# Kernel optimization log

Measured on AMD Instinct MI355X. Metric: run time of the kernel, lower is better.

## Reference

```python
import jax, jax.numpy as jnp
import numpy as np

B, N, DIM, HEADS = 8, 4096, 512, 8
BASE = 10000.0


def rope_cos_sin(n, dim, base=BASE):
    k_max = dim // 2
    theta = 1.0 / base ** (jnp.arange(k_max, dtype=jnp.float32) / k_max)
    angles = jnp.arange(n, dtype=jnp.float32)[:, None] * theta  # (n, k_max)
    return jnp.cos(angles), jnp.sin(angles)


def apply_rope(x, cos, sin):
    # x: (b, n, dim); complex pairs are interleaved (even=real, odd=imag)
    xr = x[..., 0::2]
    xi = x[..., 1::2]
    out_r = cos * xr - sin * xi
    out_i = sin * xr + cos * xi
    return jnp.stack([out_r, out_i], axis=-1).reshape(x.shape)


def setup_inputs() -> dict:
    key = jax.random.key(0)
    ks = jax.random.split(key, 8)
    s = 0.02
    return {
        'x': jax.random.normal(ks[0], (B, N, DIM), jnp.float32),
        'y': jax.random.normal(ks[1], (B, N, DIM), jnp.float32),
        'Wq': jax.random.normal(ks[2], (DIM, DIM), jnp.float32) * s,
        'bq': jax.random.normal(ks[3], (DIM,), jnp.float32) * s,
        'Wk': jax.random.normal(ks[4], (DIM, DIM), jnp.float32) * s,
        'bk': jax.random.normal(ks[5], (DIM,), jnp.float32) * s,
        'lepe_w': jax.random.normal(ks[6], (DIM, 1, 3), jnp.float32) * s,
        'lepe_b': jax.random.normal(ks[7], (DIM,), jnp.float32) * s,
    }


def reference(x, y, Wq, bq, Wk, bk, lepe_w, lepe_b):
    b, n, c = x.shape
    h = HEADS
    d = c // h
    q = jax.nn.elu(x @ Wq.T + bq) + 1.0
    k = jax.nn.elu(y @ Wk.T + bk) + 1.0
    cos, sin = rope_cos_sin(n, c)
    q_rope = apply_rope(q, cos, sin).reshape(b, n, h, d).transpose(0, 2, 1, 3)
    k_rope = apply_rope(k, cos, sin).reshape(b, n, h, d).transpose(0, 2, 1, 3)
    qh = q.reshape(b, n, h, d).transpose(0, 2, 1, 3)
    kh = k.reshape(b, n, h, d).transpose(0, 2, 1, 3)
    v = y.reshape(b, n, h, d).transpose(0, 2, 1, 3)
    kmean = kh.mean(axis=2, keepdims=True)  # (b,h,1,d)
    z = 1.0 / (jnp.einsum('bhnd,bhmd->bhnm', qh, kmean) + 1e-6)  # (b,h,n,1)
    scale = n ** (-0.5)
    kv = jnp.einsum('bhnd,bhne->bhde', k_rope * scale, v * scale)  # (b,h,d,d)
    out = jnp.einsum('bhnd,bhde->bhne', q_rope, kv) * z  # (b,h,n,d)
    out = out.transpose(0, 2, 1, 3).reshape(b, n, c)
    # LePE: depthwise conv1d over value stream
    vc = v.transpose(0, 2, 1, 3).reshape(b, n, c).transpose(0, 2, 1)  # (b,c,n)
    lepe = jax.lax.conv_general_dilated(
        vc, lepe_w, window_strides=(1,), padding=[(1, 1)],
        dimension_numbers=('NCH', 'OIH', 'NCH'), feature_group_count=c)
    lepe = lepe + lepe_b[None, :, None]
    return out + lepe.transpose(0, 2, 1)
```

## Files before the change

kernel.cpp:

```cpp
#include <hip/hip_runtime.h>

#define B_ 8
#define N_ 4096
#define C_ 512
#define H_ 8

typedef _Float16 h8  __attribute__((ext_vector_type(8)));
typedef _Float16 h4v __attribute__((ext_vector_type(4)));
typedef float    f4  __attribute__((ext_vector_type(4)));

static const size_t OFF_COS  = 0;
static const size_t OFF_SIN  = (size_t)4*1024*1024;
static const size_t OFF_KRH  = (size_t)8*1024*1024;
static const size_t OFF_YH   = (size_t)40*1024*1024;
static const size_t OFF_WQH  = (size_t)72*1024*1024;
static const size_t OFF_WKH  = (size_t)72*1024*1024 + 512*1024;
static const size_t OFF_KSUM = (size_t)73*1024*1024;
static const size_t OFF_KVG  = (size_t)73*1024*1024 + 64*1024;
static const size_t OFF_KVT  = (size_t)74*1024*1024 + 64*1024;

__device__ __forceinline__ unsigned int pack2h(float a, float b){
    union { _Float16 h[2]; unsigned int u; } x;
    x.h[0] = (_Float16)a; x.h[1] = (_Float16)b; return x.u;
}

__global__ void k_tables(float* __restrict__ cosT, float* __restrict__ sinT){
    int n = blockIdx.x, j = threadIdx.x;
    double th = exp((double)j * -0.035977892078031970);
    float ang = (float)n * (float)th;
    float s, c; sincosf(ang, &s, &c);
    cosT[n*256 + j] = c; sinT[n*256 + j] = s;
}

__global__ __launch_bounds__(256) void k_prep_y(
    const float* __restrict__ y, const float* __restrict__ Wq, const float* __restrict__ Wk,
    _Float16* __restrict__ yh, _Float16* __restrict__ Wqh, _Float16* __restrict__ Wkh)
{
    int bid = blockIdx.x;
    const float* src; _Float16* dst; size_t base;
    if (bid < 8192)      { src = y;  dst = yh;  base = (size_t)bid*2048; }
    else if (bid < 8320) { src = Wq; dst = Wqh; base = (size_t)(bid-8192)*2048; }
    else                 { src = Wk; dst = Wkh; base = (size_t)(bid-8320)*2048; }
    size_t o = base + (size_t)threadIdx.x*8;
    float4 a = *(const float4*)&src[o];
    float4 b = *(const float4*)&src[o+4];
    uint4 r; r.x = pack2h(a.x,a.y); r.y = pack2h(a.z,a.w); r.z = pack2h(b.x,b.y); r.w = pack2h(b.z,b.w);
    *(uint4*)&dst[o] = r;
}

__global__ __launch_bounds__(256) void k_prep_x(const float* __restrict__ x, _Float16* __restrict__ xh){
    size_t o = (size_t)blockIdx.x*2048 + (size_t)threadIdx.x*8;
    float4 a = *(const float4*)&x[o];
    float4 b = *(const float4*)&x[o+4];
    uint4 r; r.x = pack2h(a.x,a.y); r.y = pack2h(a.z,a.w); r.z = pack2h(b.x,b.y); r.w = pack2h(b.z,b.w);
    *(uint4*)&xh[o] = r;
}

__device__ __forceinline__ void stage_a64(const _Float16* __restrict__ g, _Float16* lds, int t){
    int r = t >> 2;
    int j = (t & 3) ^ ((r ^ (r >> 2)) & 3);
    __builtin_amdgcn_global_load_lds(
        (const __attribute__((address_space(1))) void*)(g + (size_t)r*C_ + j*8),
        (__attribute__((address_space(3))) void*)(lds + (size_t)(t & 192)*8),
        16, 0, 0);
}
__device__ __forceinline__ void stage_b128(const _Float16* __restrict__ g, _Float16* lds, int t){
#pragma unroll
    for (int i=0;i<2;++i){
        int u = i*256 + t;
        int r = u >> 2;
        int j = (u & 3) ^ ((r ^ (r >> 2)) & 3);
        __builtin_amdgcn_global_load_lds(
            (const __attribute__((address_space(1))) void*)(g + (size_t)r*C_ + j*8),
            (__attribute__((address_space(3))) void*)(lds + (size_t)(i*256 + (t & 192))*8),
            16, 0, 0);
    }
}

template<int IS_Q>
__global__ __launch_bounds__(256, 4) void k_gemm(
    const _Float16* __restrict__ A, const _Float16* __restrict__ Wh, const float* __restrict__ bias,
    const float* __restrict__ cosT, const float* __restrict__ sinT,
    _Float16* __restrict__ krh, float* __restrict__ ksum,
    const float* __restrict__ ksumIn, const _Float16* __restrict__ kvTg,
    const _Float16* __restrict__ yh, const float* __restrict__ lw, const float* __restrict__ lb,
    float* __restrict__ outp)
{
    __shared__ __align__(16) char smem[36864];
    _Float16* qrs = (_Float16*)smem;

    const int t = threadIdx.x;
    const int lane = t & 63;
    const int w = t >> 6;
    const int wm = w >> 1, wn = w & 1;
    const int col0 = blockIdx.x * 128;
    const int row0 = blockIdx.y * 64;
    const int lrow = lane & 15, lg = lane >> 4;
    const int b = row0 >> 12;

    f4 acc[2][4] = {};
    const _Float16* Ab = A  + (size_t)row0*C_;
    const _Float16* Bb = Wh + (size_t)col0*C_;
    stage_a64 (Ab,      (_Float16*)(smem),               t);
    stage_b128(Bb,      (_Float16*)(smem + 12288),       t);
    stage_a64 (Ab + 32, (_Float16*)(smem + 4096),        t);
    stage_b128(Bb + 32, (_Float16*)(smem + 12288 + 8192),t);

    const int sw = (lrow ^ (lrow >> 2)) & 3;
    const int cK = (lg ^ sw) * 8;

#pragma unroll
    for (int kk=0; kk<16; ++kk){
        if (kk < 15) asm volatile("s_waitcnt vmcnt(3)" ::: "memory");
        else         asm volatile("s_waitcnt vmcnt(0)" ::: "memory");
        __builtin_amdgcn_s_barrier();
        if (kk < 14){
            const int ss = (kk+2)%3;
            stage_a64 (Ab + (kk+2)*32, (_Float16*)(smem + ss*4096),         t);
            stage_b128(Bb + (kk+2)*32, (_Float16*)(smem + 12288 + ss*8192), t);
        }
        const int sc = kk%3;
        const _Float16* As = (const _Float16*)(smem + sc*4096);
        const _Float16* Bs = (const _Float16*)(smem + 12288 + sc*8192);
        h8 af[2], bf[4];
#pragma unroll
        for (int mi=0; mi<2; ++mi) af[mi] = *(const h8*)&As[(wm*32 + mi*16 + lrow)*32 + cK];
#pragma unroll
        for (int ni=0; ni<4; ++ni) bf[ni] = *(const h8*)&Bs[(wn*64 + ni*16 + lrow)*32 + cK];
#pragma unroll
        for (int mi=0; mi<2; ++mi)
#pragma unroll
            for (int ni=0; ni<4; ++ni)
                acc[mi][ni] = __builtin_amdgcn_mfma_f32_16x16x32_f16(af[mi], bf[ni], acc[mi][ni], 0,0,0);
    }
    __syncthreads();

    const int hcol0 = col0 + wn*64;
    float bcol[4], km[4];
#pragma unroll
    for (int ni=0; ni<4; ++ni){
        int c = hcol0 + ni*16 + lrow;
        bcol[ni] = bias[c];
        km[ni] = IS_Q ? ksumIn[b*C_ + c] * (1.0f/4096.0f) : 0.0f;
    }
    float colsum[4] = {0.f,0.f,0.f,0.f};
    float zr[2][4];
    _Float16* qw = qrs + w*2304;

#pragma unroll
    for (int mi=0; mi<2; ++mi){
        float qv[4][4];
#pragma unroll
        for (int ni=0; ni<4; ++ni)
#pragma unroll
            for (int r=0; r<4; ++r){
                float v = acc[mi][ni][r] + bcol[ni];
                qv[ni][r] = v > 0.f ? v + 1.f : __expf(v);
            }
        if constexpr (IS_Q){
#pragma unroll
            for (int r=0; r<4; ++r){
                float p = qv[0][r]*km[0] + qv[1][r]*km[1] + qv[2][r]*km[2] + qv[3][r]*km[3];
                p += __shfl_xor(p, 1); p += __shfl_xor(p, 2);
                p += __shfl_xor(p, 4); p += __shfl_xor(p, 8);
                zr[mi][r] = 1.0f / (p + 1e-6f);
            }
        } else {
#pragma unroll
            for (int ni=0; ni<4; ++ni)
                colsum[ni] += qv[ni][0]+qv[ni][1]+qv[ni][2]+qv[ni][3];
        }
#pragma unroll
        for (int ni=0; ni<4; ++ni){
            int c = hcol0 + ni*16 + lrow;
            int jj = c >> 1;
#pragma unroll
            for (int r=0; r<4; ++r){
                int grow = row0 + wm*32 + mi*16 + lg*4 + r;
                int n = grow & (N_-1);
                float val = qv[ni][r];
                float par = __shfl_xor(val, 1);
                float cs = cosT[n*256 + jj], sn = sinT[n*256 + jj];
                float rv = (lane & 1) ? fmaf(sn, par, cs*val) : fmaf(cs, val, -sn*par);
                float prv = __shfl_xor(rv, 1);
                if constexpr (IS_Q){
                    if (!(lane & 1))
                        *(unsigned int*)&qw[(mi*16 + lg*4 + r)*72 + (ni*16 + lrow)] = pack2h(rv, prv);
                } else {
                    if (!(lane & 1))
                        *(unsigned int*)&krh[(size_t)grow*C_ + c] = pack2h(rv, prv);
                }
            }
        }
    }

    if constexpr (!IS_Q){
#pragma unroll
        for (int ni=0; ni<4; ++ni){
            float s = colsum[ni];
            s += __shfl_xor(s, 16); s += __shfl_xor(s, 32);
            if (lane < 16) atomicAdd(&ksum[b*C_ + hcol0 + ni*16 + lane], s);
        }
    } else {
        const int bhh = b*H_ + (col0 >> 6) + wn;
        h8 kv0[4], kv1[4];
#pragma unroll
        for (int ni2=0; ni2<4; ++ni2){
            int e = ni2*16 + lrow;
            kv0[ni2] = *(const h8*)&kvTg[(size_t)bhh*4096 + e*64 + lg*8];
            kv1[ni2] = *(const h8*)&kvTg[(size_t)bhh*4096 + e*64 + 32 + lg*8];
        }
        __syncthreads();
        f4 acc2[2][4] = {};
#pragma unroll
        for (int mi2=0; mi2<2; ++mi2){
            h8 a0 = *(const h8*)&qw[(mi2*16 + lrow)*72 + 0*32 + lg*8];
            h8 a1 = *(const h8*)&qw[(mi2*16 + lrow)*72 + 1*32 + lg*8];
#pragma unroll
            for (int ni2=0; ni2<4; ++ni2){
                acc2[mi2][ni2] = __builtin_amdgcn_mfma_f32_16x16x32_f16(a0, kv0[ni2], acc2[mi2][ni2], 0,0,0);
                acc2[mi2][ni2] = __builtin_amdgcn_mfma_f32_16x16x32_f16(a1, kv1[ni2], acc2[mi2][ni2], 0,0,0);
            }
        }
#pragma unroll
        for (int mi2=0; mi2<2; ++mi2){
#pragma unroll
            for (int r=0; r<4; ++r){
                float z = zr[mi2][r];
#pragma unroll
                for (int ni2=0; ni2<4; ++ni2){
                    float val = acc2[mi2][ni2][r] * z;
                    float pv = __shfl_xor(val, 1);
                    if (!(lane & 1))
                        *(unsigned int*)&qw[(mi2*16 + lg*4 + r)*72 + (ni2*16 + lrow)] = pack2h(val, pv);
                }
            }
        }
        __syncthreads();
        const int cg = t & 31;
        const int c4p = cg * 4;
        const int hl = c4p >> 6;
        const int e0 = c4p & 63;
        float w0[4], w1[4], w2[4], wb[4];
#pragma unroll
        for (int j=0;j<4;++j){
            int cc = col0 + c4p + j;
            w0[j]=lw[cc*3+0]; w1[j]=lw[cc*3+1]; w2[j]=lw[cc*3+2]; wb[j]=lb[cc];
        }
#pragma unroll
        for (int i=0;i<8;++i){
            int rl = (t >> 5) + i*8;
            int grow = row0 + rl;
            int nloc = grow & (N_-1);
            int wreg = ((rl >> 5) << 1) + hl;
            h4v a = *(const h4v*)&qrs[wreg*2304 + (rl & 31)*72 + e0];
            const _Float16* yp = yh + (size_t)grow*C_ + col0 + c4p;
            h4v y1 = *(const h4v*)yp;
            float s0 = fmaf((float)y1[0], w1[0], wb[0]);
            float s1 = fmaf((float)y1[1], w1[1], wb[1]);
            float s2 = fmaf((float)y1[2], w1[2], wb[2]);
            float s3 = fmaf((float)y1[3], w1[3], wb[3]);
            if (nloc > 0){
                h4v y0 = *(const h4v*)(yp - C_);
                s0 = fmaf((float)y0[0], w0[0], s0); s1 = fmaf((float)y0[1], w0[1], s1);
                s2 = fmaf((float)y0[2], w0[2], s2); s3 = fmaf((float)y0[3], w0[3], s3);
            }
            if (nloc < N_-1){
                h4v y2 = *(const h4v*)(yp + C_);
                s0 = fmaf((float)y2[0], w2[0], s0); s1 = fmaf((float)y2[1], w2[1], s1);
                s2 = fmaf((float)y2[2], w2[2], s2); s3 = fmaf((float)y2[3], w2[3], s3);
            }
            float4 o;
            o.x = (float)a[0] + s0; o.y = (float)a[1] + s1;
            o.z = (float)a[2] + s2; o.w = (float)a[3] + s3;
            *(float4*)&outp[(size_t)grow*C_ + col0 + c4p] = o;
        }
    }
}

__global__ __launch_bounds__(256) void k_kv(const _Float16* __restrict__ krh, const _Float16* __restrict__ yh,
                                            float* __restrict__ kvg){
    __shared__ _Float16 krs[64*128];
    __shared__ _Float16 vs[64*128];
    const int split = blockIdx.x, bh = blockIdx.y;
    const int b = bh >> 3, h = bh & 7;
    const int t = threadIdx.x, lane = t & 63, w = t >> 6;
    const int lrow = lane & 15, lg = lane >> 4;
    f4 acc[4] = {};
    for (int sub=0; sub<4; ++sub){
        const int n0 = split*512 + sub*128;
#pragma unroll
        for (int i=0;i<8;++i){
            int q = i*256 + t;
            int d2 = q & 31, n2 = q >> 5;
            int n = n0 + 2*n2, c = h*64 + 2*d2;
            size_t g0 = (size_t)(b*N_ + n)*C_ + c;
            unsigned int u0 = *(const unsigned int*)&krh[g0];
            unsigned int u1 = *(const unsigned int*)&krh[g0 + C_];
            unsigned int v0 = *(const unsigned int*)&yh[g0];
            unsigned int v1 = *(const unsigned int*)&yh[g0 + C_];
            int chunk = n2 >> 2, j2 = (n2 & 3)*2;
            int pc0 = chunk ^ ((2*d2) & 15);
            int pc1 = pc0 ^ 1;
            *(unsigned int*)&krs[(2*d2)*128 + pc0*8 + j2]   = (u0 & 0xffffu) | (u1 << 16);
            *(unsigned int*)&krs[(2*d2+1)*128 + pc1*8 + j2] = (u0 >> 16) | (u1 & 0xffff0000u);
            *(unsigned int*)&vs[(2*d2)*128 + pc0*8 + j2]    = (v0 & 0xffffu) | (v1 << 16);
            *(unsigned int*)&vs[(2*d2+1)*128 + pc1*8 + j2]  = (v0 >> 16) | (v1 & 0xffff0000u);
        }
        __syncthreads();
#pragma unroll
        for (int ks=0; ks<4; ++ks){
            int cu = ((ks*4 + lg) ^ lrow)*8;
            h8 a = *(const h8*)&krs[(w*16 + lrow)*128 + cu];
#pragma unroll
            for (int ni=0; ni<4; ++ni){
                h8 bv = *(const h8*)&vs[(ni*16 + lrow)*128 + cu];
                acc[ni] = __builtin_amdgcn_mfma_f32_16x16x32_f16(a, bv, acc[ni], 0,0,0);
            }
        }
        __syncthreads();
    }
#pragma unroll
    for (int ni=0; ni<4; ++ni)
#pragma unroll
        for (int rr=0; rr<4; ++rr)
            atomicAdd(&kvg[(size_t)bh*4096 + (w*16 + lg*4 + rr)*64 + ni*16 + lrow],
                      acc[ni][rr] * (1.0f/4096.0f));
}

__global__ __launch_bounds__(256) void k_kvmerge(const float* __restrict__ kvg, _Float16* __restrict__ kvTg){
    int bh = blockIdx.x, t = threadIdx.x;
    const float* src = kvg + (size_t)bh*4096;
    _Float16* dst = kvTg + (size_t)bh*4096;
#pragma unroll
    for (int i=0;i<4;++i){
        int q = i*256 + t;
        int e2 = q & 31, d2 = q >> 5;
        float2 a0 = *(const float2*)&src[(2*d2)*64 + 2*e2];
        float2 a1 = *(const float2*)&src[(2*d2+1)*64 + 2*e2];
        *(unsigned int*)&dst[(2*e2)*64 + 2*d2]   = pack2h(a0.x, a1.x);
        *(unsigned int*)&dst[(2*e2+1)*64 + 2*d2] = pack2h(a0.y, a1.y);
    }
}

extern "C" void kernel_launch(void* const* d_in, const int* in_sizes, int n_in,
                              void* d_out, int out_size, void* d_ws, size_t ws_size,
                              hipStream_t stream)
{
    (void)in_sizes; (void)n_in; (void)out_size; (void)ws_size;
    const float* x  = (const float*)d_in[0];
    const float* y  = (const float*)d_in[1];
    const float* Wq = (const float*)d_in[2];
    const float* bq = (const float*)d_in[3];
    const float* Wk = (const float*)d_in[4];
    const float* bk = (const float*)d_in[5];
    const float* lw = (const float*)d_in[6];
    const float* lb = (const float*)d_in[7];

    char* ws = (char*)d_ws;
    float*    cosT = (float*)(ws + OFF_COS);
    float*    sinT = (float*)(ws + OFF_SIN);
    _Float16* krh  = (_Float16*)(ws + OFF_KRH);
    _Float16* yh   = (_Float16*)(ws + OFF_YH);
    _Float16* Wqh  = (_Float16*)(ws + OFF_WQH);
    _Float16* Wkh  = (_Float16*)(ws + OFF_WKH);
    float*    ksum = (float*)(ws + OFF_KSUM);
    float*    kvg  = (float*)(ws + OFF_KVG);
    _Float16* kvTg = (_Float16*)(ws + OFF_KVT);
    float*    out  = (float*)d_out;

    hipMemsetAsync(ws + OFF_KSUM, 0, 64*1024 + 1024*1024, stream);
    k_tables<<<dim3(N_), dim3(256), 0, stream>>>(cosT, sinT);
    k_prep_y<<<dim3(8448), dim3(256), 0, stream>>>(y, Wq, Wk, yh, Wqh, Wkh);
    k_gemm<0><<<dim3(4, 512), dim3(256), 0, stream>>>(yh, Wkh, bk, cosT, sinT,
        krh, ksum, nullptr, nullptr, nullptr, nullptr, nullptr, nullptr);
    k_kv<<<dim3(8, 64), dim3(256), 0, stream>>>(krh, yh, kvg);
    k_kvmerge<<<dim3(64), dim3(256), 0, stream>>>(kvg, kvTg);
    k_prep_x<<<dim3(8192), dim3(256), 0, stream>>>(x, krh);
    k_gemm<1><<<dim3(4, 512), dim3(256), 0, stream>>>(krh, Wqh, bq, cosT, sinT,
        nullptr, nullptr, ksum, kvTg, yh, lw, lb, out);
}
```

Before: 195.6 us.

## Fuse KV outer-product into K GEMM epilogue and interleave RoPE tables

The K projection GEMM now keeps its rotated K tile in shared memory, loads the matching V tile from yh, and computes the per-tile K^T V partial product with MFMA before atomically adding it to the global kv accumulator. This removes the separate k_kv kernel and the write and re-read of the rotated K buffer in global memory. The cos/sin tables are rebuilt as interleaved float2 arrays indexed by frequency then position, so each lane reads four positions with two vector loads. The x and y fp16 conversions are merged into a single prep kernel. The cost is far more atomics on kvg, one per 64-row tile instead of one per 512-row split, plus extra shared-memory and register pressure in the GEMM epilogue.

```diff
diff --git a/kernel.cpp b/kernel.cpp
--- a/kernel.cpp
+++ b/kernel.cpp
@@ -9,9 +9,8 @@
 typedef _Float16 h4v __attribute__((ext_vector_type(4)));
 typedef float    f4  __attribute__((ext_vector_type(4)));
 
-static const size_t OFF_COS  = 0;
-static const size_t OFF_SIN  = (size_t)4*1024*1024;
-static const size_t OFF_KRH  = (size_t)8*1024*1024;
+static const size_t OFF_CT   = 0;
+static const size_t OFF_XH   = (size_t)8*1024*1024;
 static const size_t OFF_YH   = (size_t)40*1024*1024;
 static const size_t OFF_WQH  = (size_t)72*1024*1024;
 static const size_t OFF_WKH  = (size_t)72*1024*1024 + 512*1024;
@@ -24,36 +23,35 @@
     x.h[0] = (_Float16)a; x.h[1] = (_Float16)b; return x.u;
 }
 
-__global__ void k_tables(float* __restrict__ cosT, float* __restrict__ sinT){
-    int n = blockIdx.x, j = threadIdx.x;
-    double th = exp((double)j * -0.035977892078031970);
-    float ang = (float)n * (float)th;
-    float s, c; sincosf(ang, &s, &c);
-    cosT[n*256 + j] = c; sinT[n*256 + j] = s;
-}
-
-__global__ __launch_bounds__(256) void k_prep_y(
-    const float* __restrict__ y, const float* __restrict__ Wq, const float* __restrict__ Wk,
-    _Float16* __restrict__ yh, _Float16* __restrict__ Wqh, _Float16* __restrict__ Wkh)
+__global__ __launch_bounds__(256) void k_tables(float2* __restrict__ ct){
+    int jj = blockIdx.x, t = threadIdx.x;
+    double th = exp((double)jj * -0.035977892078031970);
+    float thf = (float)th;
+#pragma unroll
+    for (int i=0;i<16;++i){
+        int n = i*256 + t;
+        float s, c; sincosf((float)n * thf, &s, &c);
+        ct[(size_t)jj*4096 + n] = make_float2(c, s);
+    }
+}
+
+__global__ __launch_bounds__(256) void k_prep(
+    const float* __restrict__ y, const float* __restrict__ x,
+    const float* __restrict__ Wq, const float* __restrict__ Wk,
+    _Float16* __restrict__ yh, _Float16* __restrict__ xh,
+    _Float16* __restrict__ Wqh, _Float16* __restrict__ Wkh)
 {
     int bid = blockIdx.x;
     const float* src; _Float16* dst; size_t base;
-    if (bid < 8192)      { src = y;  dst = yh;  base = (size_t)bid*2048; }
-    else if (bid < 8320) { src = Wq; dst = Wqh; base = (size_t)(bid-8192)*2048; }
-    else                 { src = Wk; dst = Wkh; base = (size_t)(bid-8320)*2048; }
+    if (bid < 8192)       { src = y;  dst = yh;  base = (size_t)bid*2048; }
+    else if (bid < 16384) { src = x;  dst = xh;  base = (size_t)(bid-8192)*2048; }
+    else if (bid < 16512) { src = Wq; dst = Wqh; base = (size_t)(bid-16384)*2048; }
+    else                  { src = Wk; dst = Wkh; base = (size_t)(bid-16512)*2048; }
     size_t o = base + (size_t)threadIdx.x*8;
     float4 a = *(const float4*)&src[o];
     float4 b = *(const float4*)&src[o+4];
     uint4 r; r.x = pack2h(a.x,a.y); r.y = pack2h(a.z,a.w); r.z = pack2h(b.x,b.y); r.w = pack2h(b.z,b.w);
     *(uint4*)&dst[o] = r;
-}
-
-__global__ __launch_bounds__(256) void k_prep_x(const float* __restrict__ x, _Float16* __restrict__ xh){
-    size_t o = (size_t)blockIdx.x*2048 + (size_t)threadIdx.x*8;
-    float4 a = *(const float4*)&x[o];
-    float4 b = *(const float4*)&x[o+4];
-    uint4 r; r.x = pack2h(a.x,a.y); r.y = pack2h(a.z,a.w); r.z = pack2h(b.x,b.y); r.w = pack2h(b.z,b.w);
-    *(uint4*)&xh[o] = r;
 }
 
 __device__ __forceinline__ void stage_a64(const _Float16* __restrict__ g, _Float16* lds, int t){
@@ -80,14 +78,16 @@
 template<int IS_Q>
 __global__ __launch_bounds__(256, 4) void k_gemm(
     const _Float16* __restrict__ A, const _Float16* __restrict__ Wh, const float* __restrict__ bias,
-    const float* __restrict__ cosT, const float* __restrict__ sinT,
-    _Float16* __restrict__ krh, float* __restrict__ ksum,
-    const float* __restrict__ ksumIn, const _Float16* __restrict__ kvTg,
+    const float2* __restrict__ ct,
+    float* __restrict__ ksum, const float* __restrict__ ksumIn,
+    float* __restrict__ kvg, const _Float16* __restrict__ kvTg,
     const _Float16* __restrict__ yh, const float* __restrict__ lw, const float* __restrict__ lb,
     float* __restrict__ outp)
 {
     __shared__ __align__(16) char smem[36864];
     _Float16* qrs = (_Float16*)smem;
+    unsigned int* krsU = (unsigned int*)smem;
+    unsigned int* vsU  = (unsigned int*)(smem + 16384);
 
     const int t = threadIdx.x;
     const int lane = t & 63;
@@ -170,26 +170,35 @@
             for (int ni=0; ni<4; ++ni)
                 colsum[ni] += qv[ni][0]+qv[ni][1]+qv[ni][2]+qv[ni][3];
         }
+        const int n0 = (row0 & (N_-1)) + wm*32 + mi*16 + lg*4;
 #pragma unroll
         for (int ni=0; ni<4; ++ni){
             int c = hcol0 + ni*16 + lrow;
             int jj = c >> 1;
+            const float4* tp = (const float4*)&ct[(size_t)jj*4096 + n0];
+            float4 ta = tp[0], tb = tp[1];
+            float cs4[4] = {ta.x, ta.z, tb.x, tb.z};
+            float sn4[4] = {ta.y, ta.w, tb.y, tb.w};
+            float rv[4];
 #pragma unroll
             for (int r=0; r<4; ++r){
-                int grow = row0 + wm*32 + mi*16 + lg*4 + r;
-                int n = grow & (N_-1);
                 float val = qv[ni][r];
                 float par = __shfl_xor(val, 1);
-                float cs = cosT[n*256 + jj], sn = sinT[n*256 + jj];
-                float rv = (lane & 1) ? fmaf(sn, par, cs*val) : fmaf(cs, val, -sn*par);
-                float prv = __shfl_xor(rv, 1);
-                if constexpr (IS_Q){
+                rv[r] = (lane & 1) ? fmaf(sn4[r], par, cs4[r]*val) : fmaf(cs4[r], val, -sn4[r]*par);
+            }
+            if constexpr (IS_Q){
+#pragma unroll
+                for (int r=0; r<4; ++r){
+                    float prv = __shfl_xor(rv[r], 1);
                     if (!(lane & 1))
-                        *(unsigned int*)&qw[(mi*16 + lg*4 + r)*72 + (ni*16 + lrow)] = pack2h(rv, prv);
-                } else {
-                    if (!(lane & 1))
-                        *(unsigned int*)&krh[(size_t)grow*C_ + c] = pack2h(rv, prv);
+                        *(unsigned int*)&qw[(mi*16 + lg*4 + r)*72 + (ni*16 + lrow)] = pack2h(rv[r], prv);
                 }
+            } else {
+                int d = ni*16 + lrow;
+                int n2 = wm*16 + mi*8 + lg*2;
+                unsigned int* p = &krsU[wn*2048 + d*32 + (n2 ^ ((d & 7) << 2))];
+                uint2 pr; pr.x = pack2h(rv[0], rv[1]); pr.y = pack2h(rv[2], rv[3]);
+                *(uint2*)p = pr;
             }
         }
     }
@@ -201,6 +210,63 @@
             s += __shfl_xor(s, 16); s += __shfl_xor(s, 32);
             if (lane < 16) atomicAdd(&ksum[b*C_ + hcol0 + ni*16 + lane], s);
         }
+        {
+            const int grp = lane >> 4, li = lane & 15;
+#pragma unroll
+            for (int it=0; it<8; ++it){
+                int g = it*4 + w;
+                int hl = g >> 4, q = g & 15;
+                int row = q*4 + grp;
+                uint2 mine = *(const uint2*)&yh[(size_t)(row0 + row)*C_ + col0 + hl*64 + li*4];
+                uint2 oth; oth.x = __shfl_xor(mine.x, 16); oth.y = __shfl_xor(mine.y, 16);
+                if (!(grp & 1)){
+                    int n2 = row >> 1;
+#pragma unroll
+                    for (int e=0; e<4; ++e){
+                        int ea = li*4 + e;
+                        unsigned int mf = ((e<2 ? mine.x : mine.y) >> ((e&1)*16)) & 0xffffu;
+                        unsigned int of = ((e<2 ? oth.x  : oth.y ) >> ((e&1)*16)) & 0xffffu;
+                        vsU[hl*2048 + ea*32 + (n2 ^ ((ea & 7) << 2))] = mf | (of << 16);
+                    }
+                }
+            }
+        }
+        __syncthreads();
+        f4 acc2[2][4] = {};
+        const unsigned int* krsW = krsU + wn*2048;
+        const unsigned int* vsW  = vsU  + wn*2048;
+#pragma unroll
+        for (int ks=0; ks<2; ++ks){
+            h8 a2[2], b2[4];
+#pragma unroll
+            for (int mi2=0; mi2<2; ++mi2){
+                int d = wm*32 + mi2*16 + lrow;
+                int c4 = (ks*16 + lg*4) ^ ((d & 7) << 2);
+                a2[mi2] = *(const h8*)&krsW[d*32 + c4];
+            }
+#pragma unroll
+            for (int ni2=0; ni2<4; ++ni2){
+                int e = ni2*16 + lrow;
+                int c4 = (ks*16 + lg*4) ^ ((e & 7) << 2);
+                b2[ni2] = *(const h8*)&vsW[e*32 + c4];
+            }
+#pragma unroll
+            for (int mi2=0; mi2<2; ++mi2)
+#pragma unroll
+                for (int ni2=0; ni2<4; ++ni2)
+                    acc2[mi2][ni2] = __builtin_amdgcn_mfma_f32_16x16x32_f16(a2[mi2], b2[ni2], acc2[mi2][ni2], 0,0,0);
+        }
+        const int bh = b*H_ + (col0 >> 6) + wn;
+#pragma unroll
+        for (int mi2=0; mi2<2; ++mi2)
+#pragma unroll
+            for (int ni2=0; ni2<4; ++ni2)
+#pragma unroll
+                for (int rr=0; rr<4; ++rr){
+                    int d = wm*32 + mi2*16 + lg*4 + rr;
+                    int e = ni2*16 + lrow;
+                    atomicAdd(&kvg[(size_t)bh*4096 + d*64 + e], acc2[mi2][ni2][rr] * (1.0f/4096.0f));
+                }
     } else {
         const int bhh = b*H_ + (col0 >> 6) + wn;
         h8 kv0[4], kv1[4];
@@ -278,56 +344,6 @@
     }
 }
 
-__global__ __launch_bounds__(256) void k_kv(const _Float16* __restrict__ krh, const _Float16* __restrict__ yh,
-                                            float* __restrict__ kvg){
-    __shared__ _Float16 krs[64*128];
-    __shared__ _Float16 vs[64*128];
-    const int split = blockIdx.x, bh = blockIdx.y;
-    const int b = bh >> 3, h = bh & 7;
-    const int t = threadIdx.x, lane = t & 63, w = t >> 6;
-    const int lrow = lane & 15, lg = lane >> 4;
-    f4 acc[4] = {};
-    for (int sub=0; sub<4; ++sub){
-        const int n0 = split*512 + sub*128;
-#pragma unroll
-        for (int i=0;i<8;++i){
-            int q = i*256 + t;
-            int d2 = q & 31, n2 = q >> 5;
-            int n = n0 + 2*n2, c = h*64 + 2*d2;
-            size_t g0 = (size_t)(b*N_ + n)*C_ + c;
-            unsigned int u0 = *(const unsigned int*)&krh[g0];
-            unsigned int u1 = *(const unsigned int*)&krh[g0 + C_];
-            unsigned int v0 = *(const unsigned int*)&yh[g0];
-            unsigned int v1 = *(const unsigned int*)&yh[g0 + C_];
-            int chunk = n2 >> 2, j2 = (n2 & 3)*2;
-            int pc0 = chunk ^ ((2*d2) & 15);
-            int pc1 = pc0 ^ 1;
-            *(unsigned int*)&krs[(2*d2)*128 + pc0*8 + j2]   = (u0 & 0xffffu) | (u1 << 16);
-            *(unsigned int*)&krs[(2*d2+1)*128 + pc1*8 + j2] = (u0 >> 16) | (u1 & 0xffff0000u);
-            *(unsigned int*)&vs[(2*d2)*128 + pc0*8 + j2]    = (v0 & 0xffffu) | (v1 << 16);
-            *(unsigned int*)&vs[(2*d2+1)*128 + pc1*8 + j2]  = (v0 >> 16) | (v1 & 0xffff0000u);
-        }
-        __syncthreads();
-#pragma unroll
-        for (int ks=0; ks<4; ++ks){
-            int cu = ((ks*4 + lg) ^ lrow)*8;
-            h8 a = *(const h8*)&krs[(w*16 + lrow)*128 + cu];
-#pragma unroll
-            for (int ni=0; ni<4; ++ni){
-                h8 bv = *(const h8*)&vs[(ni*16 + lrow)*128 + cu];
-                acc[ni] = __builtin_amdgcn_mfma_f32_16x16x32_f16(a, bv, acc[ni], 0,0,0);
-            }
-        }
-        __syncthreads();
-    }
-#pragma unroll
-    for (int ni=0; ni<4; ++ni)
-#pragma unroll
-        for (int rr=0; rr<4; ++rr)
-            atomicAdd(&kvg[(size_t)bh*4096 + (w*16 + lg*4 + rr)*64 + ni*16 + lrow],
-                      acc[ni][rr] * (1.0f/4096.0f));
-}
-
 __global__ __launch_bounds__(256) void k_kvmerge(const float* __restrict__ kvg, _Float16* __restrict__ kvTg){
     int bh = blockIdx.x, t = threadIdx.x;
     const float* src = kvg + (size_t)bh*4096;
@@ -358,9 +374,8 @@
     const float* lb = (const float*)d_in[7];
 
     char* ws = (char*)d_ws;
-    float*    cosT = (float*)(ws + OFF_COS);
-    float*    sinT = (float*)(ws + OFF_SIN);
-    _Float16* krh  = (_Float16*)(ws + OFF_KRH);
+    float2*   ct   = (float2*)(ws + OFF_CT);
+    _Float16* xh   = (_Float16*)(ws + OFF_XH);
     _Float16* yh   = (_Float16*)(ws + OFF_YH);
     _Float16* Wqh  = (_Float16*)(ws + OFF_WQH);
     _Float16* Wkh  = (_Float16*)(ws + OFF_WKH);
@@ -370,13 +385,11 @@
     float*    out  = (float*)d_out;
 
     hipMemsetAsync(ws + OFF_KSUM, 0, 64*1024 + 1024*1024, stream);
-    k_tables<<<dim3(N_), dim3(256), 0, stream>>>(cosT, sinT);
-    k_prep_y<<<dim3(8448), dim3(256), 0, stream>>>(y, Wq, Wk, yh, Wqh, Wkh);
-    k_gemm<0><<<dim3(4, 512), dim3(256), 0, stream>>>(yh, Wkh, bk, cosT, sinT,
-        krh, ksum, nullptr, nullptr, nullptr, nullptr, nullptr, nullptr);
-    k_kv<<<dim3(8, 64), dim3(256), 0, stream>>>(krh, yh, kvg);
+    k_tables<<<dim3(256), dim3(256), 0, stream>>>(ct);
+    k_prep<<<dim3(16640), dim3(256), 0, stream>>>(y, x, Wq, Wk, yh, xh, Wqh, Wkh);
+    k_gemm<0><<<dim3(4, 512), dim3(256), 0, stream>>>(yh, Wkh, bk, ct,
+        ksum, nullptr, kvg, nullptr, yh, nullptr, nullptr, nullptr);
     k_kvmerge<<<dim3(64), dim3(256), 0, stream>>>(kvg, kvTg);
-    k_prep_x<<<dim3(8192), dim3(256), 0, stream>>>(x, krh);
-    k_gemm<1><<<dim3(4, 512), dim3(256), 0, stream>>>(krh, Wqh, bq, cosT, sinT,
-        nullptr, nullptr, ksum, kvTg, yh, lw, lb, out);
-}
+    k_gemm<1><<<dim3(4, 512), dim3(256), 0, stream>>>(xh, Wqh, bq, ct,
+        nullptr, ksum, nullptr, kvTg, yh, lw, lb, out);
+}
```

Result: no change. 197.5 us (+1.0%).
